# Kernel optimization log

Hardware: AMD Instinct MI355X
Metric: run time of the kernel (lower is better)

## Reference

```python
import jax, jax.numpy as jnp
from jax import lax
import numpy as np

B, CIN, COUT, N, H, W = 16, 64, 64, 8, 128, 128


def setup_inputs() -> dict:
    key = jax.random.key(0)
    ks = jax.random.split(key, 6)
    s = 0.05
    return {
        "x": jax.random.normal(ks[0], (B, CIN, H, W), dtype=jnp.float32),
        "condition": jax.random.normal(ks[1], (B, CIN), dtype=jnp.float32),
        "filt_w": jax.random.normal(ks[2], (N, COUT, CIN, 3, 3), dtype=jnp.float32) * s,
        "filt_b": jax.random.normal(ks[3], (N, COUT), dtype=jnp.float32) * s,
        "sel_w": jax.random.normal(ks[4], (N, CIN), dtype=jnp.float32) * s,
        "sel_b": jax.random.normal(ks[5], (N,), dtype=jnp.float32) * s,
    }


def reference(x, condition, filt_w, filt_b, sel_w, sel_b):
    b = x.shape[0]
    # condition selector: Linear(in_channels -> num_conditions) + softmax
    logits = condition.reshape(b, -1) @ sel_w.T + sel_b          # [B, N]
    weights = jax.nn.softmax(logits, axis=-1)                    # [B, N]

    n, cout, cin, kh, kw = filt_w.shape
    # Run all N branch convs in ONE conv by stacking filters on the output-channel axis.
    kern = filt_w.reshape(n * cout, cin, kh, kw)
    y = lax.conv_general_dilated(
        x, kern, window_strides=(1, 1), padding="SAME",
        dimension_numbers=("NCHW", "OIHW", "NCHW"))              # [B, N*COUT, H, W]
    h, w = y.shape[-2], y.shape[-1]
    y = y.reshape(b, n, cout, h, w) + filt_b.reshape(1, n, cout, 1, 1)
    # softmax-gated sum over the N branches
    out = jnp.einsum("bn,bnohw->bohw", weights, y)
    return out
```

## Files before the change

### kernel.cpp

```cpp
#include <hip/hip_runtime.h>
#include <stdint.h>

#define BATCH 16
#define CIN   64
#define COUT  64
#define NBR   8
#define HH    128
#define WW    128


typedef __attribute__((ext_vector_type(8)))  short short8;
typedef __attribute__((ext_vector_type(16))) float f32x16;

__device__ __forceinline__ unsigned short f2bf(float f) {
    union { float f; uint32_t u; } v; v.f = f;
    uint32_t u = v.u;
    return (unsigned short)((u + 0x7FFFu + ((u >> 16) & 1u)) >> 16);
}

__global__ void k_weights(const float* __restrict__ cond,
                          const float* __restrict__ sel_w,
                          const float* __restrict__ sel_b,
                          float* __restrict__ wt) {
    __shared__ float lg[BATCH][NBR];
    int t = threadIdx.x;
    int b = t >> 3, n = t & 7;
    float acc = sel_b[n];
    #pragma unroll
    for (int c = 0; c < CIN; ++c)
        acc += cond[b * CIN + c] * sel_w[n * CIN + c];
    lg[b][n] = acc;
    __syncthreads();
    float m = -1e30f;
    #pragma unroll
    for (int i = 0; i < NBR; ++i) m = fmaxf(m, lg[b][i]);
    float s = 0.f;
    #pragma unroll
    for (int i = 0; i < NBR; ++i) s += __expf(lg[b][i] - m);
    wt[t] = __expf(lg[b][n] - m) / s;
}

__global__ void k_combine(const float* __restrict__ filt_w,
                          const float* __restrict__ filt_b,
                          const float* __restrict__ wt,
                          unsigned short* __restrict__ wfilt,
                          float* __restrict__ cbias) {
    const int NF = BATCH * 9 * COUT * CIN;
    int idx = blockIdx.x * 256 + threadIdx.x;
    if (idx < NF) {
        int c  = idx & 63;
        int o  = (idx >> 6) & 63;
        int bt = idx >> 12;
        int t  = bt % 9;
        int b  = bt / 9;
        float acc = 0.f;
        #pragma unroll
        for (int n = 0; n < NBR; ++n)
            acc += wt[b * NBR + n] * filt_w[((n * COUT + o) * CIN + c) * 9 + t];
        wfilt[idx] = f2bf(acc);
    } else {
        int j = idx - NF;
        if (j < BATCH * COUT) {
            int b = j >> 6, o = j & 63;
            float acc = 0.f;
            #pragma unroll
            for (int n = 0; n < NBR; ++n)
                acc += wt[b * NBR + n] * filt_b[n * COUT + o];
            cbias[j] = acc;
        }
    }
}

#define RT 8
#define WT 32
#define SLABW 34
#define SLABR 10
#define PSTR  68

__device__ __forceinline__ short8 lds_frag(const unsigned short* p) {
    union { uint2 u[2]; short8 s; } t;
    t.u[0] = *(const uint2*)p;
    t.u[1] = *(const uint2*)(p + 4);
    return t.s;
}
__device__ __forceinline__ short8 gld_frag(const unsigned short* p) {
    union { uint4 u; short8 s; } t;
    t.u = *(const uint4*)p;
    return t.s;
}

__global__ __launch_bounds__(256)
void k_conv(const float* __restrict__ x,
            const unsigned short* __restrict__ wfilt,
            const float* __restrict__ cbias,
            float* __restrict__ out) {
    __shared__ unsigned short lx[SLABR * SLABW * PSTR];
    __shared__ float lbias[COUT];

    const int b  = blockIdx.z;
    const int h0 = blockIdx.y * RT;
    const int w0 = blockIdx.x * WT;
    const int tid = threadIdx.x;

    if (tid < COUT) lbias[tid] = cbias[b * COUT + tid];

    const int NTASK = SLABR * SLABW * 8;
    for (int task = tid; task < NTASK; task += 256) {
        int wc  = task % SLABW;
        int pos = task / SLABW;
        int s   = pos % SLABR;
        int cg  = pos / SLABR;
        int hin = h0 + s - 1;
        int win = w0 + wc - 1;
        unsigned short v[8];
        if (hin >= 0 && hin < HH && win >= 0 && win < WW) {
            const float* px = x + (((long)(b * CIN + cg * 8) * HH + hin) * WW + win);
            #pragma unroll
            for (int j = 0; j < 8; ++j) v[j] = f2bf(px[(long)j * HH * WW]);
        } else {
            #pragma unroll
            for (int j = 0; j < 8; ++j) v[j] = 0;
        }
        int base = (s * SLABW + wc) * PSTR + cg * 8;
        uint2 lo, hi;
        lo.x = (unsigned)v[0] | ((unsigned)v[1] << 16);
        lo.y = (unsigned)v[2] | ((unsigned)v[3] << 16);
        hi.x = (unsigned)v[4] | ((unsigned)v[5] << 16);
        hi.y = (unsigned)v[6] | ((unsigned)v[7] << 16);
        *(uint2*)&lx[base]     = lo;
        *(uint2*)&lx[base + 4] = hi;
    }
    __syncthreads();

    const int lane = tid & 63;
    const int wave = tid >> 6;
    const int l31  = lane & 31;
    const int lh   = lane >> 5;
    const int r0   = wave * 2;

    f32x16 acc00, acc01, acc10, acc11;
    #pragma unroll
    for (int i = 0; i < 16; ++i) { acc00[i] = 0.f; acc01[i] = 0.f; acc10[i] = 0.f; acc11[i] = 0.f; }

    const unsigned short* wf = wfilt + (long)b * 9 * COUT * CIN;

    #pragma unroll
    for (int tap = 0; tap < 9; ++tap) {
        const int kh = tap / 3, kw = tap % 3;
        const unsigned short* wft = wf + (long)tap * COUT * CIN;
        #pragma unroll
        for (int cc = 0; cc < 4; ++cc) {
            const int kofs = cc * 16 + lh * 8;
            short8 a0 = gld_frag(wft + (l31)      * CIN + kofs);
            short8 a1 = gld_frag(wft + (32 + l31) * CIN + kofs);
            short8 b0 = lds_frag(&lx[((r0     + kh) * SLABW + l31 + kw) * PSTR + kofs]);
            short8 b1 = lds_frag(&lx[((r0 + 1 + kh) * SLABW + l31 + kw) * PSTR + kofs]);
            acc00 = __builtin_amdgcn_mfma_f32_32x32x16_bf16(a0, b0, acc00, 0, 0, 0);
            acc01 = __builtin_amdgcn_mfma_f32_32x32x16_bf16(a0, b1, acc01, 0, 0, 0);
            acc10 = __builtin_amdgcn_mfma_f32_32x32x16_bf16(a1, b0, acc10, 0, 0, 0);
            acc11 = __builtin_amdgcn_mfma_f32_32x32x16_bf16(a1, b1, acc11, 0, 0, 0);
        }
    }

    #pragma unroll
    for (int cb = 0; cb < 2; ++cb) {
        #pragma unroll
        for (int pb = 0; pb < 2; ++pb) {
            const f32x16 v = cb == 0 ? (pb == 0 ? acc00 : acc01)
                                     : (pb == 0 ? acc10 : acc11);
            const int hrow = h0 + r0 + pb;
            float* op = out + (((long)(b * COUT + cb * 32) * HH + hrow) * WW + w0 + l31);
            #pragma unroll
            for (int i = 0; i < 16; ++i) {
                int m = (i & 3) + 8 * (i >> 2) + 4 * lh;
                op[(long)m * HH * WW] = v[i] + lbias[cb * 32 + m];
            }
        }
    }
}

extern "C" void kernel_launch(void* const* d_in, const int* in_sizes, int n_in,
                              void* d_out, int out_size, void* d_ws, size_t ws_size,
                              hipStream_t stream) {
    const float* x      = (const float*)d_in[0];
    const float* cond   = (const float*)d_in[1];
    const float* filt_w = (const float*)d_in[2];
    const float* filt_b = (const float*)d_in[3];
    const float* sel_w  = (const float*)d_in[4];
    const float* sel_b  = (const float*)d_in[5];
    float* out = (float*)d_out;

    float* wt             = (float*)d_ws;
    float* cbias          = (float*)((char*)d_ws + 512);
    unsigned short* wfilt = (unsigned short*)((char*)d_ws + 4608);

    k_weights<<<1, 128, 0, stream>>>(cond, sel_w, sel_b, wt);

    const int NF = BATCH * 9 * COUT * CIN + BATCH * COUT;
    k_combine<<<(NF + 255) / 256, 256, 0, stream>>>(filt_w, filt_b, wt, wfilt, cbias);

    dim3 grid(WW / WT, HH / RT, BATCH);
    k_conv<<<grid, 256, 0, stream>>>(x, wfilt, cbias, out);
}
```

Baseline: 196.4 us.

## Pre-transpose input to padded channel-last bf16 and load conv operands from global

Merges the softmax-weight and filter-combine kernels into one prep kernel, where each thread computes all 9 taps. Adds a transpose kernel that writes x as a zero-padded NHWC bf16 tensor in workspace. The conv kernel then reads its B fragments straight from global memory, with no LDS staging or sync, and starts the accumulators at the bias. This adds a full extra pass over x and a larger workspace requirement, with a fallback to the old kernel when the workspace is too small.

```diff
diff --git a/kernel.cpp b/kernel.cpp
--- a/kernel.cpp
+++ b/kernel.cpp
@@ -7,7 +7,7 @@
 #define NBR   8
 #define HH    128
 #define WW    128
-
+#define HP    130
 
 typedef __attribute__((ext_vector_type(8)))  short short8;
 typedef __attribute__((ext_vector_type(16))) float f32x16;
@@ -17,56 +17,168 @@
     uint32_t u = v.u;
     return (unsigned short)((u + 0x7FFFu + ((u >> 16) & 1u)) >> 16);
 }
-
-__global__ void k_weights(const float* __restrict__ cond,
-                          const float* __restrict__ sel_w,
-                          const float* __restrict__ sel_b,
-                          float* __restrict__ wt) {
+__device__ __forceinline__ short8 gld_frag(const unsigned short* p) {
+    union { uint4 u; short8 s; } t;
+    t.u = *(const uint4*)p;
+    return t.s;
+}
+
+__global__ __launch_bounds__(256)
+void k_prep(const float* __restrict__ cond,
+            const float* __restrict__ sel_w,
+            const float* __restrict__ sel_b,
+            const float* __restrict__ filt_w,
+            const float* __restrict__ filt_b,
+            unsigned short* __restrict__ wfilt,
+            float* __restrict__ cbias) {
     __shared__ float lg[BATCH][NBR];
-    int t = threadIdx.x;
-    int b = t >> 3, n = t & 7;
-    float acc = sel_b[n];
-    #pragma unroll
-    for (int c = 0; c < CIN; ++c)
-        acc += cond[b * CIN + c] * sel_w[n * CIN + c];
-    lg[b][n] = acc;
+    const int tid = threadIdx.x;
+    if (tid < BATCH * NBR) {
+        int b2 = tid >> 3, n = tid & 7;
+        float acc = sel_b[n];
+        #pragma unroll
+        for (int c = 0; c < CIN; ++c)
+            acc += cond[b2 * CIN + c] * sel_w[n * CIN + c];
+        lg[b2][n] = acc;
+    }
     __syncthreads();
-    float m = -1e30f;
-    #pragma unroll
-    for (int i = 0; i < NBR; ++i) m = fmaxf(m, lg[b][i]);
-    float s = 0.f;
-    #pragma unroll
-    for (int i = 0; i < NBR; ++i) s += __expf(lg[b][i] - m);
-    wt[t] = __expf(lg[b][n] - m) / s;
-}
-
-__global__ void k_combine(const float* __restrict__ filt_w,
-                          const float* __restrict__ filt_b,
-                          const float* __restrict__ wt,
-                          unsigned short* __restrict__ wfilt,
-                          float* __restrict__ cbias) {
-    const int NF = BATCH * 9 * COUT * CIN;
-    int idx = blockIdx.x * 256 + threadIdx.x;
-    if (idx < NF) {
-        int c  = idx & 63;
-        int o  = (idx >> 6) & 63;
-        int bt = idx >> 12;
-        int t  = bt % 9;
-        int b  = bt / 9;
-        float acc = 0.f;
-        #pragma unroll
-        for (int n = 0; n < NBR; ++n)
-            acc += wt[b * NBR + n] * filt_w[((n * COUT + o) * CIN + c) * 9 + t];
-        wfilt[idx] = f2bf(acc);
+
+    const int idx = blockIdx.x * 256 + tid;
+    const int b  = idx >> 12;
+    const int oc = idx & 4095;
+    const int o  = oc >> 6, c = oc & 63;
+
+    float w8[NBR];
+    {
+        float m = -1e30f;
+        #pragma unroll
+        for (int n = 0; n < NBR; ++n) m = fmaxf(m, lg[b][n]);
+        float s = 0.f;
+        #pragma unroll
+        for (int n = 0; n < NBR; ++n) { w8[n] = __expf(lg[b][n] - m); s += w8[n]; }
+        float inv = 1.f / s;
+        #pragma unroll
+        for (int n = 0; n < NBR; ++n) w8[n] *= inv;
+    }
+
+    float acc[9];
+    #pragma unroll
+    for (int t = 0; t < 9; ++t) acc[t] = 0.f;
+    #pragma unroll
+    for (int n = 0; n < NBR; ++n) {
+        const float* p = filt_w + ((long)(n * COUT + o) * CIN + c) * 9;
+        #pragma unroll
+        for (int t = 0; t < 9; ++t) acc[t] += w8[n] * p[t];
+    }
+    #pragma unroll
+    for (int t = 0; t < 9; ++t)
+        wfilt[((long)(b * 9 + t) * 4096) + oc] = f2bf(acc[t]);
+
+    if (oc < COUT) {
+        float ab = 0.f;
+        #pragma unroll
+        for (int n = 0; n < NBR; ++n) ab += w8[n] * filt_b[n * COUT + oc];
+        cbias[b * COUT + oc] = ab;
+    }
+}
+
+__global__ __launch_bounds__(256)
+void k_xpose(const float* __restrict__ x, unsigned short* __restrict__ x_t) {
+    const int b = blockIdx.y;
+    const int idx = blockIdx.x * 256 + threadIdx.x;
+    if (idx >= HP * HP) return;
+    const int h = idx / HP, w = idx % HP;
+    const bool interior = (h >= 1) & (h <= HH) & (w >= 1) & (w <= WW);
+    unsigned short* dst = x_t + ((long)(b * HP + h) * HP + w) * CIN;
+
+    if (interior) {
+        const float* src = x + ((long)b * CIN * HH + (h - 1)) * WW + (w - 1);
+        #pragma unroll
+        for (int half = 0; half < 2; ++half) {
+            float v[32];
+            #pragma unroll
+            for (int c = 0; c < 32; ++c)
+                v[c] = src[(long)(half * 32 + c) * HH * WW];
+            uint4 q[4];
+            #pragma unroll
+            for (int j = 0; j < 4; ++j) {
+                q[j].x = (unsigned)f2bf(v[8*j+0]) | ((unsigned)f2bf(v[8*j+1]) << 16);
+                q[j].y = (unsigned)f2bf(v[8*j+2]) | ((unsigned)f2bf(v[8*j+3]) << 16);
+                q[j].z = (unsigned)f2bf(v[8*j+4]) | ((unsigned)f2bf(v[8*j+5]) << 16);
+                q[j].w = (unsigned)f2bf(v[8*j+6]) | ((unsigned)f2bf(v[8*j+7]) << 16);
+            }
+            #pragma unroll
+            for (int j = 0; j < 4; ++j)
+                ((uint4*)dst)[half * 4 + j] = q[j];
+        }
     } else {
-        int j = idx - NF;
-        if (j < BATCH * COUT) {
-            int b = j >> 6, o = j & 63;
-            float acc = 0.f;
-            #pragma unroll
-            for (int n = 0; n < NBR; ++n)
-                acc += wt[b * NBR + n] * filt_b[n * COUT + o];
-            cbias[j] = acc;
+        uint4 z; z.x = z.y = z.z = z.w = 0;
+        #pragma unroll
+        for (int j = 0; j < 8; ++j) ((uint4*)dst)[j] = z;
+    }
+}
+
+__global__ __launch_bounds__(256)
+void k_conv2(const unsigned short* __restrict__ x_t,
+             const unsigned short* __restrict__ wfilt,
+             const float* __restrict__ cbias,
+             float* __restrict__ out) {
+    const int b  = blockIdx.z;
+    const int h0 = blockIdx.y * 8;
+    const int w0 = blockIdx.x * 32;
+    const int tid  = threadIdx.x;
+    const int lane = tid & 63;
+    const int wave = tid >> 6;
+    const int l31  = lane & 31;
+    const int lh   = lane >> 5;
+    const int r0   = wave * 2;
+
+    f32x16 acc00, acc01, acc10, acc11;
+    #pragma unroll
+    for (int i = 0; i < 16; ++i) {
+        const int m = (i & 3) + 8 * (i >> 2) + 4 * lh;
+        const float b0 = cbias[b * COUT + m];
+        const float b1 = cbias[b * COUT + 32 + m];
+        acc00[i] = b0; acc01[i] = b0;
+        acc10[i] = b1; acc11[i] = b1;
+    }
+
+    const unsigned short* wf = wfilt + (long)b * 9 * COUT * CIN;
+    const unsigned short* xb = x_t + (long)b * HP * HP * CIN;
+
+    #pragma unroll
+    for (int tap = 0; tap < 9; ++tap) {
+        const int kh = tap / 3, kw = tap % 3;
+        const unsigned short* row0 = xb + ((long)(h0 + r0 + kh) * HP + (w0 + kw + l31)) * CIN;
+        const unsigned short* row1 = row0 + (long)HP * CIN;
+        const unsigned short* wft  = wf + (long)tap * COUT * CIN;
+        #pragma unroll
+        for (int cc = 0; cc < 4; ++cc) {
+            const int kofs = cc * 16 + lh * 8;
+            short8 a0 = gld_frag(wft + l31 * CIN + kofs);
+            short8 a1 = gld_frag(wft + (32 + l31) * CIN + kofs);
+            short8 b0 = gld_frag(row0 + kofs);
+            short8 b1 = gld_frag(row1 + kofs);
+            acc00 = __builtin_amdgcn_mfma_f32_32x32x16_bf16(a0, b0, acc00, 0, 0, 0);
+            acc01 = __builtin_amdgcn_mfma_f32_32x32x16_bf16(a0, b1, acc01, 0, 0, 0);
+            acc10 = __builtin_amdgcn_mfma_f32_32x32x16_bf16(a1, b0, acc10, 0, 0, 0);
+            acc11 = __builtin_amdgcn_mfma_f32_32x32x16_bf16(a1, b1, acc11, 0, 0, 0);
+        }
+    }
+
+    #pragma unroll
+    for (int cb = 0; cb < 2; ++cb) {
+        #pragma unroll
+        for (int pb = 0; pb < 2; ++pb) {
+            const f32x16 v = cb == 0 ? (pb == 0 ? acc00 : acc01)
+                                     : (pb == 0 ? acc10 : acc11);
+            const int hrow = h0 + r0 + pb;
+            float* op = out + (((long)(b * COUT + cb * 32) * HH + hrow) * WW + w0 + l31);
+            #pragma unroll
+            for (int i = 0; i < 16; ++i) {
+                const int m = (i & 3) + 8 * (i >> 2) + 4 * lh;
+                op[(long)m * HH * WW] = v[i];
+            }
         }
     }
 }
@@ -83,17 +195,12 @@
     t.u[1] = *(const uint2*)(p + 4);
     return t.s;
 }
-__device__ __forceinline__ short8 gld_frag(const unsigned short* p) {
-    union { uint4 u; short8 s; } t;
-    t.u = *(const uint4*)p;
-    return t.s;
-}
 
 __global__ __launch_bounds__(256)
-void k_conv(const float* __restrict__ x,
-            const unsigned short* __restrict__ wfilt,
-            const float* __restrict__ cbias,
-            float* __restrict__ out) {
+void k_conv_fb(const float* __restrict__ x,
+               const unsigned short* __restrict__ wfilt,
+               const float* __restrict__ cbias,
+               float* __restrict__ out) {
     __shared__ unsigned short lx[SLABR * SLABW * PSTR];
     __shared__ float lbias[COUT];
 
@@ -190,15 +297,20 @@
     const float* sel_b  = (const float*)d_in[5];
     float* out = (float*)d_out;
 
-    float* wt             = (float*)d_ws;
-    float* cbias          = (float*)((char*)d_ws + 512);
-    unsigned short* wfilt = (unsigned short*)((char*)d_ws + 4608);
-
-    k_weights<<<1, 128, 0, stream>>>(cond, sel_w, sel_b, wt);
-
-    const int NF = BATCH * 9 * COUT * CIN + BATCH * COUT;
-    k_combine<<<(NF + 255) / 256, 256, 0, stream>>>(filt_w, filt_b, wt, wfilt, cbias);
-
-    dim3 grid(WW / WT, HH / RT, BATCH);
-    k_conv<<<grid, 256, 0, stream>>>(x, wfilt, cbias, out);
-}
+    float*          cbias = (float*)d_ws;
+    unsigned short* wfilt = (unsigned short*)((char*)d_ws + 4096);
+    unsigned short* x_t   = (unsigned short*)((char*)d_ws + 1183744);
+    const size_t need = 1183744ull + (size_t)BATCH * HP * HP * CIN * 2ull;
+
+    k_prep<<<256, 256, 0, stream>>>(cond, sel_w, sel_b, filt_w, filt_b, wfilt, cbias);
+
+    if (ws_size >= need) {
+        dim3 gx((HP * HP + 255) / 256, BATCH);
+        k_xpose<<<gx, 256, 0, stream>>>(x, x_t);
+        dim3 grid(WW / 32, HH / 8, BATCH);
+        k_conv2<<<grid, 256, 0, stream>>>(x_t, wfilt, cbias, out);
+    } else {
+        dim3 grid(WW / WT, HH / RT, BATCH);
+        k_conv_fb<<<grid, 256, 0, stream>>>(x, wfilt, cbias, out);
+    }
+}
```

Measured after the change: 210.7 us. +7.3%, slower.
